# Kernel tuning notes

Hardware: AMD Instinct MI355X
Metric: run time of the kernel (lower is better)

## Reference

```python
import jax, jax.numpy as jnp
import numpy as np

N = 50000          # num nodes
E = 800000         # num edges
DIN = 128          # in_channels
C = 64             # out_channels per head
H = 2              # heads
ED = 32            # edge_dim


def setup_inputs() -> dict:
    key = jax.random.key(0)
    ks = jax.random.split(key, 12)
    s = 1.0 / np.sqrt(DIN)
    se = 1.0 / np.sqrt(ED)
    return {
        "x": jax.random.normal(ks[0], (N, DIN), dtype=jnp.float32),
        "edge_index": jax.random.randint(ks[1], (2, E), 0, N, dtype=jnp.int32),
        "edge_attr": jax.random.normal(ks[2], (E, ED), dtype=jnp.float32),
        "Wq": jax.random.uniform(ks[3], (DIN, H * C), jnp.float32, -s, s),
        "bq": jax.random.uniform(ks[4], (H * C,), jnp.float32, -s, s),
        "Wk": jax.random.uniform(ks[5], (DIN, H * C), jnp.float32, -s, s),
        "bk": jax.random.uniform(ks[6], (H * C,), jnp.float32, -s, s),
        "Wv": jax.random.uniform(ks[7], (DIN, H * C), jnp.float32, -s, s),
        "bv": jax.random.uniform(ks[8], (H * C,), jnp.float32, -s, s),
        "We": jax.random.uniform(ks[9], (ED, H * C), jnp.float32, -se, se),
        "Wskip": jax.random.uniform(ks[10], (DIN, H * C), jnp.float32, -s, s),
        "bskip": jax.random.uniform(ks[11], (H * C,), jnp.float32, -s, s),
    }


def reference(x, edge_index, edge_attr, Wq, bq, Wk, bk, Wv, bv, We, Wskip, bskip):
    src, dst = edge_index[0], edge_index[1]
    # node-level projections [N, H, C]
    q = (x @ Wq + bq).reshape(N, H, C)
    k = (x @ Wk + bk).reshape(N, H, C)
    v = (x @ Wv + bv).reshape(N, H, C)
    e = (edge_attr @ We).reshape(E, H, C)  # lin_edge, no bias

    # per-edge gather
    q_e = q[dst]              # [E, H, C]
    k_e = k[src] + e          # key gets edge features
    alpha = jnp.einsum("ehc,ehc->eh", q_e, k_e) / jnp.sqrt(jnp.float32(C))

    # segment softmax over incoming edges of each dst node
    m = jax.ops.segment_max(alpha, dst, num_segments=N)       # [N, H]
    alpha = jnp.exp(alpha - m[dst])
    denom = jax.ops.segment_sum(alpha, dst, num_segments=N)   # [N, H]
    alpha = alpha / (denom[dst] + 1e-16)

    # weighted aggregation of values (value also gets edge features)
    msg = (v[src] + e) * alpha[..., None]                     # [E, H, C]
    out = jax.ops.segment_sum(msg, dst, num_segments=N)       # [N, H, C]
    out = out.reshape(N, H * C)

    # root weight skip connection (concat=True, beta=False)
    return out + x @ Wskip + bskip
```

## Files before the change

### kernel.cpp

```cpp
#include <hip/hip_runtime.h>
#include <cstdint>

#define NN 50000
#define EE 800000
#define DINC 128
#define HC 128
#define EDC 32
#define CAP 56
#define TILES 1563
#define SCAT_BLKS 3125
#define NB_SCAN 196

typedef __attribute__((ext_vector_type(8))) short short8;
typedef __attribute__((ext_vector_type(4))) float floatx4;

__device__ __forceinline__ unsigned int pk2(float a, float b){
  unsigned int ua = __float_as_uint(a), ub = __float_as_uint(b);
  ua = (ua + 0x7FFFu + ((ua >> 16) & 1u)) >> 16;
  ub = (ub + 0x7FFFu + ((ub >> 16) & 1u)) & 0xFFFF0000u;
  return ua | ub;
}
__device__ __forceinline__ float bflo(unsigned int p){ return __uint_as_float(p << 16); }
__device__ __forceinline__ float bfhi(unsigned int p){ return __uint_as_float(p & 0xFFFF0000u); }

__global__ __launch_bounds__(256) void k_prew(
    const float* __restrict__ Wq, const float* __restrict__ Wk,
    const float* __restrict__ Wv, const float* __restrict__ Wsk,
    unsigned int* __restrict__ Wp)
{
  int idx = blockIdx.x*256 + threadIdx.x;
  int mat = idx >> 13;
  int r   = idx & 8191;
  int kp  = r >> 7;
  int n   = r & 127;
  const float* W = (mat==0)?Wq:(mat==1)?Wk:(mat==2)?Wv:Wsk;
  Wp[(mat<<13) + n*64 + kp] = pk2(W[(2*kp)*HC + n], W[(2*kp+1)*HC + n]);
}

__global__ __launch_bounds__(256) void k_fused(
    const float* __restrict__ x, const unsigned int* __restrict__ Wp,
    const float* __restrict__ bq, const float* __restrict__ bk,
    const float* __restrict__ bv, const float* __restrict__ bsk,
    const int* __restrict__ ei,
    unsigned int* __restrict__ qbf, unsigned int* __restrict__ kvb,
    float* __restrict__ out, int* __restrict__ cnt, int* __restrict__ eidl,
    const int do_scatter)
{
  __shared__ unsigned int sx[32*68];
  __shared__ float facc[32*132];

  if (do_scatter && blockIdx.x >= TILES){
    int e = (blockIdx.x - TILES)*256 + threadIdx.x;
    if (e < EE){
      int d = ei[EE + e];
      int pos = atomicAdd(cnt + d, 1);
      if (pos < CAP) eidl[d*CAP + pos] = e;
    }
    return;
  }

  const int tid = threadIdx.x;
  const int bm  = blockIdx.x * 32;

  for (int idx = tid; idx < 32*32; idx += 256){
    int row = idx >> 5, kq = idx & 31;
    int gr = bm + row;
    unsigned int p0 = 0u, p1 = 0u;
    if (gr < NN){
      float4 v = *(const float4*)(x + (size_t)gr*DINC + 4*kq);
      p0 = pk2(v.x, v.y); p1 = pk2(v.z, v.w);
    }
    sx[row*68 + 2*kq]     = p0;
    sx[row*68 + 2*kq + 1] = p1;
  }
  __syncthreads();

  const int l = tid & 63, wid = tid >> 6;
  const int lm = l & 15, ks = l >> 4;
  const int n0 = wid * 32;

  #pragma unroll
  for (int mat = 0; mat < 4; ++mat){
    const unsigned int* wp = Wp + (mat<<13);
    const float* bi = (mat==0)?bq:(mat==1)?bk:(mat==2)?bv:bsk;

    floatx4 acc[2][2];
    #pragma unroll
    for (int mt=0;mt<2;mt++)
      #pragma unroll
      for (int nt=0;nt<2;nt++) acc[mt][nt] = (floatx4){0.f,0.f,0.f,0.f};

    #pragma unroll
    for (int kb = 0; kb < 4; ++kb){
      short8 a0 = *(const short8*)(sx + lm*68        + kb*16 + ks*4);
      short8 a1 = *(const short8*)(sx + (16+lm)*68   + kb*16 + ks*4);
      short8 b0 = *(const short8*)(wp + (n0+lm)*64    + kb*16 + ks*4);
      short8 b1 = *(const short8*)(wp + (n0+16+lm)*64 + kb*16 + ks*4);
      acc[0][0] = __builtin_amdgcn_mfma_f32_16x16x32_bf16(a0, b0, acc[0][0], 0, 0, 0);
      acc[0][1] = __builtin_amdgcn_mfma_f32_16x16x32_bf16(a0, b1, acc[0][1], 0, 0, 0);
      acc[1][0] = __builtin_amdgcn_mfma_f32_16x16x32_bf16(a1, b0, acc[1][0], 0, 0, 0);
      acc[1][1] = __builtin_amdgcn_mfma_f32_16x16x32_bf16(a1, b1, acc[1][1], 0, 0, 0);
    }
    __syncthreads();

    #pragma unroll
    for (int mt=0;mt<2;mt++)
      #pragma unroll
      for (int nt=0;nt<2;nt++)
        #pragma unroll
        for (int r=0;r<4;r++){
          int row = mt*16 + ks*4 + r;
          int col = n0 + nt*16 + lm;
          facc[row*132 + col] = acc[mt][nt][r];
        }
    __syncthreads();

    for (int idx = tid; idx < 32*64; idx += 256){
      int row = idx >> 6, cp = idx & 63;
      int gr = bm + row;
      if (gr >= NN) continue;
      float2 vv = *(const float2*)(facc + row*132 + 2*cp);
      float2 bb = *(const float2*)(bi + 2*cp);
      float v0 = vv.x + bb.x, v1 = vv.y + bb.y;
      if (mat == 0)      qbf[gr*64 + cp] = pk2(v0, v1);
      else if (mat == 1) kvb[(size_t)gr*128 + cp]      = pk2(v0, v1);
      else if (mat == 2) kvb[(size_t)gr*128 + 64 + cp] = pk2(v0, v1);
      else *(float2*)(out + (size_t)gr*HC + 2*cp) = make_float2(v0, v1);
    }
  }
}

__global__ __launch_bounds__(256) void k_count(const int* __restrict__ ei,
    int* __restrict__ cnt)
{
  int e = blockIdx.x*256 + threadIdx.x;
  if (e < EE) atomicAdd(cnt + ei[EE + e], 1);
}
__global__ __launch_bounds__(256) void k_blksum(const int* __restrict__ cnt,
    int* __restrict__ bsum)
{
  __shared__ int s[256];
  int t = threadIdx.x, i = blockIdx.x*256 + t;
  s[t] = (i < NN) ? cnt[i] : 0;
  __syncthreads();
  for (int d = 128; d > 0; d >>= 1){
    if (t < d) s[t] += s[t + d];
    __syncthreads();
  }
  if (t == 0) bsum[blockIdx.x] = s[0];
}
__global__ __launch_bounds__(256) void k_bscan(const int* __restrict__ bsum,
    int* __restrict__ bpre)
{
  __shared__ int s[256];
  int t = threadIdx.x;
  int v = (t < NB_SCAN) ? bsum[t] : 0;
  s[t] = v;
  __syncthreads();
  for (int d = 1; d < 256; d <<= 1){
    int u = (t >= d) ? s[t - d] : 0;
    __syncthreads();
    s[t] += u;
    __syncthreads();
  }
  if (t < NB_SCAN) bpre[t] = s[t] - v;
}
__global__ __launch_bounds__(256) void k_scan3(const int* __restrict__ cnt,
    const int* __restrict__ bpre, int* __restrict__ off, int* __restrict__ woff)
{
  __shared__ int s[256];
  int t = threadIdx.x, i = blockIdx.x*256 + t;
  int v = (i < NN) ? cnt[i] : 0;
  s[t] = v;
  __syncthreads();
  for (int d = 1; d < 256; d <<= 1){
    int u = (t >= d) ? s[t - d] : 0;
    __syncthreads();
    s[t] += u;
    __syncthreads();
  }
  if (i < NN){
    int o = bpre[blockIdx.x] + s[t] - v;
    off[i] = o; woff[i] = o;
  }
}
__global__ __launch_bounds__(256) void k_scatter(const int* __restrict__ ei,
    int* __restrict__ woff, int* __restrict__ eidl)
{
  int e = blockIdx.x*256 + threadIdx.x;
  if (e < EE){
    int d = ei[EE + e];
    int pos = atomicAdd(woff + d, 1);
    eidl[pos] = e;
  }
}

__global__ __launch_bounds__(256) void k_agg(
    const float* __restrict__ eattr, const float* __restrict__ We,
    const unsigned int* __restrict__ qbf, const unsigned int* __restrict__ kvb,
    const int* __restrict__ ei,
    const int* __restrict__ cnt, const int* __restrict__ off,
    const int* __restrict__ eidl, const int fixed,
    float* __restrict__ out)
{
  __shared__ float sWeT[128*33];
  __shared__ float sWea[256];
  const int tid = threadIdx.x;
  for (int idx = tid; idx < EDC*HC; idx += 256){
    int jj = idx >> 7, col = idx & 127;
    sWeT[col*33 + jj] = We[idx];
  }
  __syncthreads();

  const int wid = tid >> 6, l = tid & 63;
  const int node = blockIdx.x*4 + wid;
  const int h = l >> 5, j = l & 31;

  int deg = cnt[node]; if (deg > CAP) deg = CAP;
  const size_t beg = fixed ? (size_t)node*CAP : (size_t)off[node];
  int eidL = 0, srcL = 0;
  if (deg > 0){
    eidL = eidl[beg + ((l < deg) ? l : 0)];
    srcL = ei[eidL];
  }
  const unsigned int eaOff = (unsigned int)eidL * (EDC*4);
  const unsigned int kOff  = (unsigned int)srcL * 512u;
  const unsigned int jB = (unsigned int)j * 4u;
  const unsigned int lB = (unsigned int)l * 4u;
  const char* eac = (const char*)eattr;
  const char* kvc = (const char*)kvb;

  unsigned int qp = qbf[node*64 + l];
  float q0 = bflo(qp), q1 = bfhi(qp);
  float Pl = 0.f;
  {
    const uint4* qrow4 = (const uint4*)(qbf + node*64 + h*32);
    const float* wt = sWeT + (h*64)*33 + j;
    #pragma unroll
    for (int c4 = 0; c4 < 8; ++c4){
      uint4 u = qrow4[c4];
      int b = 8*c4;
      Pl += bflo(u.x)*wt[(b+0)*33] + bfhi(u.x)*wt[(b+1)*33];
      Pl += bflo(u.y)*wt[(b+2)*33] + bfhi(u.y)*wt[(b+3)*33];
      Pl += bflo(u.z)*wt[(b+4)*33] + bfhi(u.z)*wt[(b+5)*33];
      Pl += bflo(u.w)*wt[(b+6)*33] + bfhi(u.w)*wt[(b+7)*33];
    }
  }

#define GATHER(base, EA, KK, VV)                                 \
  {                                                              \
    _Pragma("unroll")                                            \
    for (int t = 0; t < 4; ++t){                                 \
      int s = (base) + t;                                        \
      int it = (s < deg) ? s : 0;                                \
      unsigned int eo = (unsigned int)__shfl((int)eaOff, it, 64) + jB; \
      unsigned int ko = (unsigned int)__shfl((int)kOff,  it, 64) + lB; \
      EA[t] = *(const float*)(eac + eo);                         \
      KK[t] = *(const unsigned int*)(kvc + ko);                  \
      VV[t] = *(const unsigned int*)(kvc + ko + 256);            \
    }                                                            \
  }

  float acc0=0.f, acc1=0.f, wea=0.f, den=0.f;
  if (deg > 0){
    float eav[4]; unsigned int kk[4], vv[4];
    GATHER(0, eav, kk, vv);

    for (int i = 0; i < deg; i += 4){
      float eavn[4]; unsigned int kkn[4], vvn[4];
      const int inext = i + 4;
      if (inext < deg){
        GATHER(inext, eavn, kkn, vvn);
      }
      float p[4];
      #pragma unroll
      for (int t = 0; t < 4; ++t)
        p[t] = q0*bflo(kk[t]) + q1*bfhi(kk[t]) + Pl*eav[t];
      #pragma unroll
      for (int s = 1; s < 32; s <<= 1){
        #pragma unroll
        for (int t = 0; t < 4; ++t) p[t] += __shfl_xor(p[t], s, 32);
      }
      const int nb = deg - i;
      #pragma unroll
      for (int t = 0; t < 4; ++t){
        float a = __expf(p[t] * 0.125f);
        if (t > 0) a = (t < nb) ? a : 0.f;
        den  += a;
        acc0 += a*bflo(vv[t]);
        acc1 += a*bfhi(vv[t]);
        wea  += a*eav[t];
      }
      #pragma unroll
      for (int t = 0; t < 4; ++t){ eav[t] = eavn[t]; kk[t] = kkn[t]; vv[t] = vvn[t]; }
    }
  }
#undef GATHER

  sWea[tid] = wea;
  __syncthreads();
  float rden = 1.0f/(den + 1e-16f);
  float e0 = 0.f, e1 = 0.f;
  const float* w0 = sWeT + (2*l)*33;
  const float* w1 = sWeT + (2*l+1)*33;
  const float* wv = sWea + wid*64 + h*32;
  #pragma unroll
  for (int jj = 0; jj < 32; jj += 4){
    float4 w4 = *(const float4*)(wv + jj);
    e0 += w4.x*w0[jj]; e1 += w4.x*w1[jj];
    e0 += w4.y*w0[jj+1]; e1 += w4.y*w1[jj+1];
    e0 += w4.z*w0[jj+2]; e1 += w4.z*w1[jj+2];
    e0 += w4.w*w0[jj+3]; e1 += w4.w*w1[jj+3];
  }
  float2 sk = *(const float2*)(out + (size_t)node*HC + 2*l);
  float2 o;
  o.x = sk.x + (acc0 + e0)*rden;
  o.y = sk.y + (acc1 + e1)*rden;
  *(float2*)(out + (size_t)node*HC + 2*l) = o;
}

extern "C" void kernel_launch(void* const* d_in, const int* in_sizes, int n_in,
                              void* d_out, int out_size, void* d_ws, size_t ws_size,
                              hipStream_t stream)
{
  const float* x   = (const float*)d_in[0];
  const int*   ei  = (const int*)d_in[1];
  const float* ea  = (const float*)d_in[2];
  const float* Wq  = (const float*)d_in[3];
  const float* bq  = (const float*)d_in[4];
  const float* Wk  = (const float*)d_in[5];
  const float* bk  = (const float*)d_in[6];
  const float* Wv  = (const float*)d_in[7];
  const float* bv  = (const float*)d_in[8];
  const float* We  = (const float*)d_in[9];
  const float* Wsk = (const float*)d_in[10];
  const float* bsk = (const float*)d_in[11];
  float* out = (float*)d_out;

  char* ws = (char*)d_ws;
  unsigned int* qbf = (unsigned int*)(ws);
  unsigned int* kvb = (unsigned int*)(ws + 12800000);
  int* cnt = (int*)(ws + 38400000);

  hipMemsetAsync(cnt, 0, NN*sizeof(int), stream);

  if (ws_size >= 50000000ull){
    int* eidl = (int*)(ws + 38600000);
    unsigned int* Wp = (unsigned int*)(ws + 49800064);
    k_prew<<<128, 256, 0, stream>>>(Wq, Wk, Wv, Wsk, Wp);
    k_fused<<<TILES + SCAT_BLKS, 256, 0, stream>>>(
        x, Wp, bq, bk, bv, bsk, ei, qbf, kvb, out, cnt, eidl, 1);
    k_agg<<<12500, 256, 0, stream>>>(ea, We, qbf, kvb, ei,
                                     cnt, (const int*)nullptr, eidl, 1, out);
  } else {
    int* off  = (int*)(ws + 38600000);
    int* woff = (int*)(ws + 38800000);
    int* bsum = (int*)(ws + 39000000);
    int* bpre = (int*)(ws + 39001024);
    int* eidl = (int*)(ws + 39002048);
    unsigned int* Wp = (unsigned int*)(ws + 42202112);
    k_prew<<<128, 256, 0, stream>>>(Wq, Wk, Wv, Wsk, Wp);
    k_fused<<<TILES, 256, 0, stream>>>(
        x, Wp, bq, bk, bv, bsk, ei, qbf, kvb, out, cnt, nullptr, 0);
    k_count  <<<SCAT_BLKS, 256, 0, stream>>>(ei, cnt);
    k_blksum <<<NB_SCAN, 256, 0, stream>>>(cnt, bsum);
    k_bscan  <<<1, 256, 0, stream>>>(bsum, bpre);
    k_scan3  <<<NB_SCAN, 256, 0, stream>>>(cnt, bpre, off, woff);
    k_scatter<<<SCAT_BLKS, 256, 0, stream>>>(ei, woff, eidl);
    k_agg<<<12500, 256, 0, stream>>>(ea, We, qbf, kvb, ei,
                                     cnt, off, eidl, 0, out);
  }
}
```

Baseline: 411.5 us.

## Split wave into two half-waves processing alternate edges with wider per-lane loads

Reorganizes the per-node edge aggregation so each half of the 64-lane wave handles a different edge. Within a half, 16 lanes per head each load 8-byte chunks of key, value and edge attributes, which cuts the dot-product reduction to 4 shuffle steps. The softmax scale and log2(e) are folded into q and the edge projection so exp2 can be used directly. The halves are merged with cross-half shuffles before the edge-weight projection and the vectorized output write. This trades extra combine shuffles and idle half-lanes during the final write for fewer reduction shuffles and fewer memory instructions per edge.

```diff
diff --git a/kernel.cpp b/kernel.cpp
--- a/kernel.cpp
+++ b/kernel.cpp
@@ -214,7 +214,9 @@
 
   const int wid = tid >> 6, l = tid & 63;
   const int node = blockIdx.x*4 + wid;
-  const int h = l >> 5, j = l & 31;
+  const int hf = l >> 5;
+  const int h  = (l >> 4) & 1;
+  const int g  = l & 15;
 
   int deg = cnt[node]; if (deg > CAP) deg = CAP;
   const size_t beg = fixed ? (size_t)node*CAP : (size_t)off[node];
@@ -225,17 +227,26 @@
   }
   const unsigned int eaOff = (unsigned int)eidL * (EDC*4);
   const unsigned int kOff  = (unsigned int)srcL * 512u;
-  const unsigned int jB = (unsigned int)j * 4u;
-  const unsigned int lB = (unsigned int)l * 4u;
+  const unsigned int laneK = (unsigned int)(h*128 + 8*g);
+  const unsigned int laneE = (unsigned int)(8*g);
   const char* eac = (const char*)eattr;
   const char* kvc = (const char*)kvb;
 
-  unsigned int qp = qbf[node*64 + l];
-  float q0 = bflo(qp), q1 = bfhi(qp);
-  float Pl = 0.f;
+  const float SC = 0.18033688f;
+
+  float q4[4];
   {
-    const uint4* qrow4 = (const uint4*)(qbf + node*64 + h*32);
-    const float* wt = sWeT + (h*64)*33 + j;
+    uint2 qa = *(const uint2*)(qbf + node*64 + h*32 + 2*g);
+    q4[0] = bflo(qa.x)*SC; q4[1] = bfhi(qa.x)*SC;
+    q4[2] = bflo(qa.y)*SC; q4[3] = bfhi(qa.y)*SC;
+  }
+
+  float Pl0, Pl1;
+  {
+    const int hq = l >> 5, j = l & 31;
+    const uint4* qrow4 = (const uint4*)(qbf + node*64 + hq*32);
+    const float* wt = sWeT + (hq*64)*33 + j;
+    float Pl = 0.f;
     #pragma unroll
     for (int c4 = 0; c4 < 8; ++c4){
       uint4 u = qrow4[c4];
@@ -245,78 +256,95 @@
       Pl += bflo(u.z)*wt[(b+4)*33] + bfhi(u.z)*wt[(b+5)*33];
       Pl += bflo(u.w)*wt[(b+6)*33] + bfhi(u.w)*wt[(b+7)*33];
     }
-  }
-
-#define GATHER(base, EA, KK, VV)                                 \
-  {                                                              \
-    _Pragma("unroll")                                            \
-    for (int t = 0; t < 4; ++t){                                 \
-      int s = (base) + t;                                        \
-      int it = (s < deg) ? s : 0;                                \
-      unsigned int eo = (unsigned int)__shfl((int)eaOff, it, 64) + jB; \
-      unsigned int ko = (unsigned int)__shfl((int)kOff,  it, 64) + lB; \
-      EA[t] = *(const float*)(eac + eo);                         \
-      KK[t] = *(const unsigned int*)(kvc + ko);                  \
-      VV[t] = *(const unsigned int*)(kvc + ko + 256);            \
-    }                                                            \
-  }
-
-  float acc0=0.f, acc1=0.f, wea=0.f, den=0.f;
+    Pl *= SC;
+    Pl0 = __shfl(Pl, h*32 + 2*g,     64);
+    Pl1 = __shfl(Pl, h*32 + 2*g + 1, 64);
+  }
+
+#define GATHER(base, EA, KK, VV)                                       \
+  { _Pragma("unroll")                                                  \
+    for (int t = 0; t < 2; ++t){                                       \
+      int it = (base) + 2*t + hf;                                      \
+      it = (it < deg) ? it : 0;                                        \
+      unsigned int eo = (unsigned int)__shfl((int)eaOff, it, 64) + laneE; \
+      unsigned int ko = (unsigned int)__shfl((int)kOff,  it, 64) + laneK; \
+      EA[t] = *(const float2*)(eac + eo);                              \
+      KK[t] = *(const uint2*)(kvc + ko);                               \
+      VV[t] = *(const uint2*)(kvc + ko + 256);                         \
+    } }
+
+  float acc4[4] = {0.f,0.f,0.f,0.f};
+  float wea0 = 0.f, wea1 = 0.f, den = 0.f;
   if (deg > 0){
-    float eav[4]; unsigned int kk[4], vv[4];
-    GATHER(0, eav, kk, vv);
+    float2 ea[2]; uint2 kk[2], vv[2];
+    GATHER(0, ea, kk, vv);
 
     for (int i = 0; i < deg; i += 4){
-      float eavn[4]; unsigned int kkn[4], vvn[4];
-      const int inext = i + 4;
-      if (inext < deg){
-        GATHER(inext, eavn, kkn, vvn);
-      }
-      float p[4];
-      #pragma unroll
-      for (int t = 0; t < 4; ++t)
-        p[t] = q0*bflo(kk[t]) + q1*bfhi(kk[t]) + Pl*eav[t];
-      #pragma unroll
-      for (int s = 1; s < 32; s <<= 1){
-        #pragma unroll
-        for (int t = 0; t < 4; ++t) p[t] += __shfl_xor(p[t], s, 32);
-      }
-      const int nb = deg - i;
-      #pragma unroll
-      for (int t = 0; t < 4; ++t){
-        float a = __expf(p[t] * 0.125f);
-        if (t > 0) a = (t < nb) ? a : 0.f;
-        den  += a;
-        acc0 += a*bflo(vv[t]);
-        acc1 += a*bfhi(vv[t]);
-        wea  += a*eav[t];
+      float2 ean[2]; uint2 kkn[2], vvn[2];
+      if (i + 4 < deg){
+        GATHER(i+4, ean, kkn, vvn);
       }
       #pragma unroll
-      for (int t = 0; t < 4; ++t){ eav[t] = eavn[t]; kk[t] = kkn[t]; vv[t] = vvn[t]; }
+      for (int t = 0; t < 2; ++t){
+        float p = q4[0]*bflo(kk[t].x) + q4[1]*bfhi(kk[t].x)
+                + q4[2]*bflo(kk[t].y) + q4[3]*bfhi(kk[t].y)
+                + Pl0*ea[t].x + Pl1*ea[t].y;
+        p += __shfl_xor(p, 1, 64);
+        p += __shfl_xor(p, 2, 64);
+        p += __shfl_xor(p, 4, 64);
+        p += __shfl_xor(p, 8, 64);
+        float a = __builtin_amdgcn_exp2f(p);
+        int idxe = i + 2*t + hf;
+        a = (idxe < deg) ? a : 0.f;
+        den  += a;
+        acc4[0] += a*bflo(vv[t].x); acc4[1] += a*bfhi(vv[t].x);
+        acc4[2] += a*bflo(vv[t].y); acc4[3] += a*bfhi(vv[t].y);
+        wea0 += a*ea[t].x; wea1 += a*ea[t].y;
+      }
+      #pragma unroll
+      for (int t = 0; t < 2; ++t){ ea[t] = ean[t]; kk[t] = kkn[t]; vv[t] = vvn[t]; }
     }
   }
 #undef GATHER
 
-  sWea[tid] = wea;
-  __syncthreads();
+  den += __shfl_xor(den, 32, 64);
+  #pragma unroll
+  for (int c = 0; c < 4; ++c) acc4[c] += __shfl_xor(acc4[c], 32, 64);
+  wea0 += __shfl_xor(wea0, 32, 64);
+  wea1 += __shfl_xor(wea1, 32, 64);
+
+  if (hf == 0){
+    sWea[wid*64 + h*32 + 2*g]     = wea0;
+    sWea[wid*64 + h*32 + 2*g + 1] = wea1;
+  }
+  __syncthreads();
+
   float rden = 1.0f/(den + 1e-16f);
   float e0 = 0.f, e1 = 0.f;
-  const float* w0 = sWeT + (2*l)*33;
-  const float* w1 = sWeT + (2*l+1)*33;
-  const float* wv = sWea + wid*64 + h*32;
-  #pragma unroll
-  for (int jj = 0; jj < 32; jj += 4){
-    float4 w4 = *(const float4*)(wv + jj);
-    e0 += w4.x*w0[jj]; e1 += w4.x*w1[jj];
-    e0 += w4.y*w0[jj+1]; e1 += w4.y*w1[jj+1];
-    e0 += w4.z*w0[jj+2]; e1 += w4.z*w1[jj+2];
-    e0 += w4.w*w0[jj+3]; e1 += w4.w*w1[jj+3];
-  }
-  float2 sk = *(const float2*)(out + (size_t)node*HC + 2*l);
-  float2 o;
-  o.x = sk.x + (acc0 + e0)*rden;
-  o.y = sk.y + (acc1 + e1)*rden;
-  *(float2*)(out + (size_t)node*HC + 2*l) = o;
+  {
+    const float* wrow = sWea + wid*64 + h*32;
+    const int colA = h*64 + 4*g + 2*hf;
+    const float* w0 = sWeT + colA*33;
+    const float* w1 = w0 + 33;
+    #pragma unroll
+    for (int jj = 0; jj < 32; jj += 4){
+      float4 w4 = *(const float4*)(wrow + jj);
+      e0 += w4.x*w0[jj]   + w4.y*w0[jj+1] + w4.z*w0[jj+2] + w4.w*w0[jj+3];
+      e1 += w4.x*w1[jj]   + w4.y*w1[jj+1] + w4.z*w1[jj+2] + w4.w*w1[jj+3];
+    }
+  }
+  float e2 = __shfl_xor(e0, 32, 64);
+  float e3 = __shfl_xor(e1, 32, 64);
+
+  if (hf == 0){
+    float4 sk = *(const float4*)(out + (size_t)node*HC + h*64 + 4*g);
+    float4 o;
+    o.x = sk.x + (acc4[0] + e0)*rden;
+    o.y = sk.y + (acc4[1] + e1)*rden;
+    o.z = sk.z + (acc4[2] + e2)*rden;
+    o.w = sk.w + (acc4[3] + e3)*rden;
+    *(float4*)(out + (size_t)node*HC + h*64 + 4*g) = o;
+  }
 }
 
 extern "C" void kernel_launch(void* const* d_in, const int* in_sizes, int n_in,
```

Result: slower. 431.0 us (+4.7%).
